# Kernel tuning notes

Hardware: AMD Instinct MI355X
Metric: run time of the kernel (lower is better)

## Reference

```python
import jax, jax.numpy as jnp
import numpy as np

B, C, H, W = 8, 128, 128, 128
C5 = 5 * C


def setup_inputs() -> dict:
    key = jax.random.key(0)
    ks = jax.random.split(key, 9)
    s_dw = 0.1   # depthwise weight scale
    s_pw = 0.02  # pointwise weight scale
    return {
        "x": jax.random.normal(ks[0], (B, C, H, W), jnp.float32),
        "w1": jax.random.normal(ks[1], (C5, 1, 1, 1), jnp.float32) * s_dw,
        "b1": jax.random.normal(ks[2], (C5,), jnp.float32) * 0.01,
        "w2": jax.random.normal(ks[3], (C5, 1, 3, 3), jnp.float32) * s_dw,
        "b2": jax.random.normal(ks[4], (C5,), jnp.float32) * 0.01,
        "w3": jax.random.normal(ks[5], (C5, 1, 3, 3), jnp.float32) * s_dw,
        "b3": jax.random.normal(ks[6], (C5,), jnp.float32) * 0.01,
        "w4": jax.random.normal(ks[7], (C, C5, 1, 1), jnp.float32) * s_pw,
        "b4": jax.random.normal(ks[8], (C,), jnp.float32) * 0.01,
    }


def nnstacking(x):
    # pad H,W by 1 then stack the 4-neighborhood + center along channels -> 5C
    p = jnp.pad(x, ((0, 0), (0, 0), (1, 1), (1, 1)))
    return jnp.concatenate(
        [p[:, :, 2:, 1:-1],   # neighbor below (i+1, j)
         p[:, :, :-2, 1:-1],  # neighbor above (i-1, j)
         p[:, :, 1:-1, 2:],   # neighbor right (i, j+1)
         p[:, :, 1:-1, :-2],  # neighbor left  (i, j-1)
         p[:, :, 1:-1, 1:-1]],  # center
        axis=1)


def _conv(x, w, b, dilation, padding, groups):
    y = jax.lax.conv_general_dilated(
        x, w, window_strides=(1, 1),
        padding=[(padding, padding), (padding, padding)],
        rhs_dilation=(dilation, dilation),
        dimension_numbers=("NCHW", "OIHW", "NCHW"),
        feature_group_count=groups)
    return y + b[None, :, None, None]


def reference(x, w1, b1, w2, b2, w3, b3, w4, b4):
    shortcut = x
    s = nnstacking(x)  # (B, 5C, H, W)
    # three depthwise branches (groups = 5C): 1x1 rate-1, 3x3 dil-8, 3x3 dil-12
    y = (_conv(s, w1, b1, 1, 0, C5)
         + _conv(s, w2, b2, 8, 8, C5)
         + _conv(s, w3, b3, 12, 12, C5))
    # pointwise 5C -> C, then residual add
    return _conv(y, w4, b4, 1, 0, 1) + shortcut
```

## Files before the change

kernel.cpp:

```cpp
#include <hip/hip_runtime.h>
#include <stdint.h>
#include <stddef.h>


static constexpr int Cc  = 128;
static constexpr int C5  = 640;
static constexpr int Hh  = 128;
static constexpr int Ww  = 128;
static constexpr int LC  = 160;
static constexpr int GR  = 48;
static constexpr int PSz = GR * LC + 8;

typedef __attribute__((ext_vector_type(8))) short short8;
typedef __attribute__((ext_vector_type(4))) float f32x4;

__device__ __forceinline__ uint16_t f2bf(float f) {
  uint32_t b = __float_as_uint(f);
  b += 0x7fffu + ((b >> 16) & 1u);
  return (uint16_t)(b >> 16);
}
__device__ __forceinline__ float bflo(uint32_t v) { return __uint_as_float(v << 16); }
__device__ __forceinline__ float bfhi(uint32_t v) { return __uint_as_float(v & 0xffff0000u); }

__device__ __forceinline__ void async16(uint16_t* lds, const uint16_t* gm) {
  __builtin_amdgcn_global_load_lds(
      (const __attribute__((address_space(1))) uint32_t*)gm,
      (__attribute__((address_space(3))) uint32_t*)lds, 16, 0, 0);
}

__global__ void prep_kernel(const float* __restrict__ w1, const float* __restrict__ b1,
                            const float* __restrict__ w2, const float* __restrict__ b2,
                            const float* __restrict__ w3, const float* __restrict__ b3,
                            const float* __restrict__ w4,
                            uint16_t* __restrict__ w4b, float* __restrict__ cw2,
                            float* __restrict__ cw3, float* __restrict__ bsum) {
  int i = blockIdx.x * 256 + threadIdx.x;
  if (i < Cc * C5) w4b[i] = f2bf(w4[i]);
  if (i < C5) {
    bsum[i] = b1[i] + b2[i] + b3[i];
#pragma unroll
    for (int t = 0; t < 9; ++t) {
      float a = w2[i * 9 + t];
      if (t == 4) a += w1[i] + w3[i * 9 + 4];
      cw2[i * 9 + t] = a;
      cw3[i * 9 + t] = w3[i * 9 + t];
    }
  }
}

__global__ __launch_bounds__(256, 2) void dw_kernel(
    const float* __restrict__ x, const float* __restrict__ cw2,
    const float* __restrict__ cw3, const float* __restrict__ bsum,
    uint16_t* __restrict__ y, int b0) {
  __shared__ uint16_t xs[4 * PSz];

  const int band = blockIdx.x;
  const int g    = blockIdx.y;
  const int bl   = blockIdx.z;
  const int bb   = b0 + bl;
  const int i0   = band * 16;
  const int tid  = threadIdx.x;

#pragma unroll
  for (int it = 0; it < 30; ++it) {
    int idx  = it * 256 + tid;
    int col4 = idx % 40;
    int rr   = (idx / 40) % 48;
    int cel  = idx / 1920;
    int gi = i0 - 16 + rr;
    int gj = col4 * 4 - 16;
    float4 v = make_float4(0.f, 0.f, 0.f, 0.f);
    if ((unsigned)gi < 128u && col4 >= 4 && col4 < 36) {
      v = *(const float4*)(x + (((size_t)(bb * Cc + g * 4 + cel) * Hh + gi) << 7) + gj);
    }
    ushort4 h;
    h.x = f2bf(v.x); h.y = f2bf(v.y); h.z = f2bf(v.z); h.w = f2bf(v.w);
    *(ushort4*)(xs + cel * PSz + rr * LC + col4 * 4) = h;
  }
  __syncthreads();

  const int ce = tid & 3;
  const int jt = (tid >> 2) & 7;
  const int ir = tid >> 5;
  const int j0 = jt * 16;
  const int c  = g * 4 + ce;

  float rb[48];
#define LOAD_RB(ROW)                                                      \
  do {                                                                    \
    const uint16_t* _p = xs + ce * PSz + (ROW) * LC + j0;                 \
    _Pragma("unroll") for (int _u = 0; _u < 6; ++_u) {                    \
      uint4 _q = *(const uint4*)(_p + _u * 8);                            \
      rb[_u * 8 + 0] = bflo(_q.x); rb[_u * 8 + 1] = bfhi(_q.x);           \
      rb[_u * 8 + 2] = bflo(_q.y); rb[_u * 8 + 3] = bfhi(_q.y);           \
      rb[_u * 8 + 4] = bflo(_q.z); rb[_u * 8 + 5] = bfhi(_q.z);           \
      rb[_u * 8 + 6] = bflo(_q.w); rb[_u * 8 + 7] = bfhi(_q.w);           \
    }                                                                     \
  } while (0)

  {
    float w2r[3][9], w3r[3][9], bs[3];
    const int msA[3] = {4, 2, 3};
#pragma unroll
    for (int mi = 0; mi < 3; ++mi) {
      int k = msA[mi] * Cc + c;
#pragma unroll
      for (int t = 0; t < 9; ++t) {
        w2r[mi][t] = cw2[k * 9 + t];
        w3r[mi][t] = cw3[k * 9 + t];
      }
      bs[mi] = bsum[k];
    }

#pragma unroll
    for (int it2 = 0; it2 < 2; ++it2) {
      const int i     = i0 + ir + 8 * it2;
      const int rbase = ir + 8 * it2 + 16;
      float acc[3][16];
#pragma unroll
      for (int mi = 0; mi < 3; ++mi)
#pragma unroll
        for (int jj = 0; jj < 16; ++jj) acc[mi][jj] = bs[mi];

#define AROW3(DLT, WARR, UB, DD)                                          \
      do {                                                                \
        LOAD_RB(rbase + (DLT));                                           \
        _Pragma("unroll") for (int mi = 0; mi < 3; ++mi) {                \
          const int aj = (mi == 0) ? 0 : ((mi == 1) ? 1 : -1);            \
          _Pragma("unroll") for (int v = 0; v < 3; ++v) {                 \
            const float w = WARR[mi][(UB) + v];                           \
            const int e = 16 + (DD) * (v - 1) + aj;                       \
            _Pragma("unroll") for (int jj = 0; jj < 16; ++jj)             \
              acc[mi][jj] += w * rb[e + jj];                              \
          }                                                               \
        }                                                                 \
      } while (0)

      AROW3(-12, w3r, 0, 12);
      if (j0 == 0)   acc[1][11] -= w3r[1][0] * rb[16];
      if (j0 == 112) acc[2][4]  -= w3r[2][2] * rb[31];

      AROW3(-8, w2r, 0, 8);
      if (j0 == 0)   acc[1][7]  -= w2r[1][0] * rb[16];
      if (j0 == 112) acc[2][8]  -= w2r[2][2] * rb[31];

      {
        LOAD_RB(rbase);
#pragma unroll
        for (int mi = 0; mi < 3; ++mi) {
          const int aj = (mi == 0) ? 0 : ((mi == 1) ? 1 : -1);
#pragma unroll
          for (int v = 0; v < 3; ++v) {
            const float w = w2r[mi][3 + v];
            const int e = 16 + 8 * (v - 1) + aj;
#pragma unroll
            for (int jj = 0; jj < 16; ++jj) acc[mi][jj] += w * rb[e + jj];
          }
          {
            const float w = w3r[mi][3]; const int e = 4 + aj;
#pragma unroll
            for (int jj = 0; jj < 16; ++jj) acc[mi][jj] += w * rb[e + jj];
          }
          {
            const float w = w3r[mi][5]; const int e = 28 + aj;
#pragma unroll
            for (int jj = 0; jj < 16; ++jj) acc[mi][jj] += w * rb[e + jj];
          }
        }
        if (j0 == 0)   { acc[1][7] -= w2r[1][3] * rb[16]; acc[1][11] -= w3r[1][3] * rb[16]; }
        if (j0 == 112) { acc[2][8] -= w2r[2][5] * rb[31]; acc[2][4]  -= w3r[2][5] * rb[31]; }
      }

      AROW3(8, w2r, 6, 8);
      if (j0 == 0)   acc[1][7]  -= w2r[1][6] * rb[16];
      if (j0 == 112) acc[2][8]  -= w2r[2][8] * rb[31];

      AROW3(12, w3r, 6, 12);
      if (j0 == 0)   acc[1][11] -= w3r[1][6] * rb[16];
      if (j0 == 112) acc[2][4]  -= w3r[2][8] * rb[31];
#undef AROW3

#pragma unroll
      for (int mi = 0; mi < 3; ++mi) {
        const int msA_[3] = {4, 2, 3};
        int k4 = msA_[mi] * 32 + g;
        size_t base = (((size_t)(bl * 160 + k4) << 14) + (size_t)i * Ww + j0) * 4 + ce;
#pragma unroll
        for (int jj = 0; jj < 16; ++jj) y[base + jj * 4] = f2bf(acc[mi][jj]);
      }
    }
  }

  {
    float w2r[2][9], w3r[2][9], bs[2];
#pragma unroll
    for (int mi = 0; mi < 2; ++mi) {
      int k = mi * Cc + c;
#pragma unroll
      for (int t = 0; t < 9; ++t) {
        w2r[mi][t] = cw2[k * 9 + t];
        w3r[mi][t] = cw3[k * 9 + t];
      }
      bs[mi] = bsum[k];
    }

#pragma unroll
    for (int it2 = 0; it2 < 2; ++it2) {
      const int i     = i0 + ir + 8 * it2;
      const int rbase = ir + 8 * it2 + 16;
      float acc[2][16];
#pragma unroll
      for (int mi = 0; mi < 2; ++mi)
#pragma unroll
        for (int jj = 0; jj < 16; ++jj) acc[mi][jj] = bs[mi];

#define BROW3(MI, DLT, WARR, UB, DD, BADROW)                              \
      do {                                                                \
        LOAD_RB(rbase + (DLT));                                           \
        const float sel = ((i + (DLT)) == (BADROW)) ? 0.f : 1.f;          \
        _Pragma("unroll") for (int v = 0; v < 3; ++v) {                   \
          const float w = WARR[MI][(UB) + v] * sel;                       \
          const int e = 16 + (DD) * (v - 1);                              \
          _Pragma("unroll") for (int jj = 0; jj < 16; ++jj)               \
            acc[MI][jj] += w * rb[e + jj];                                \
        }                                                                 \
      } while (0)

#define BROWC(MI, DLT, BADROW)                                            \
      do {                                                                \
        LOAD_RB(rbase + (DLT));                                           \
        const float sel = ((i + (DLT)) == (BADROW)) ? 0.f : 1.f;          \
        _Pragma("unroll") for (int v = 0; v < 3; ++v) {                   \
          const float w = w2r[MI][3 + v] * sel;                           \
          const int e = 16 + 8 * (v - 1);                                 \
          _Pragma("unroll") for (int jj = 0; jj < 16; ++jj)               \
            acc[MI][jj] += w * rb[e + jj];                                \
        }                                                                 \
        {                                                                 \
          const float w = w3r[MI][3] * sel;                               \
          _Pragma("unroll") for (int jj = 0; jj < 16; ++jj)               \
            acc[MI][jj] += w * rb[4 + jj];                                \
        }                                                                 \
        {                                                                 \
          const float w = w3r[MI][5] * sel;                               \
          _Pragma("unroll") for (int jj = 0; jj < 16; ++jj)               \
            acc[MI][jj] += w * rb[28 + jj];                               \
        }                                                                 \
      } while (0)

      BROW3(0, -11, w3r, 0, 12, 0);
      BROW3(0, -7,  w2r, 0, 8, 0);
      BROWC(0, 1, 0);
      BROW3(0, 9,   w2r, 6, 8, 0);
      BROW3(0, 13,  w3r, 6, 12, 0);
      BROW3(1, -13, w3r, 0, 12, 127);
      BROW3(1, -9,  w2r, 0, 8, 127);
      BROWC(1, -1, 127);
      BROW3(1, 7,   w2r, 6, 8, 127);
      BROW3(1, 11,  w3r, 6, 12, 127);
#undef BROW3
#undef BROWC

#pragma unroll
      for (int mi = 0; mi < 2; ++mi) {
        int k4 = mi * 32 + g;
        size_t base = (((size_t)(bl * 160 + k4) << 14) + (size_t)i * Ww + j0) * 4 + ce;
#pragma unroll
        for (int jj = 0; jj < 16; ++jj) y[base + jj * 4] = f2bf(acc[mi][jj]);
      }
    }
  }
#undef LOAD_RB
}

__global__ __launch_bounds__(256, 2) void gemm_kernel(
    const uint16_t* __restrict__ w4b, const uint16_t* __restrict__ y,
    const float* __restrict__ x, const float* __restrict__ b4,
    float* __restrict__ out, int b0) {
  __shared__ uint16_t As[128 * 64];
  __shared__ uint16_t Bs[16 * 128 * 4];

  const int tid  = threadIdx.x;
  const int lane = tid & 63;
  const int wave = tid >> 6;
  const int p0   = blockIdx.x * 128;
  const int bl   = blockIdx.y;
  const int bb   = b0 + bl;

  const int col = lane & 15;
  const int q   = lane >> 4;
  const int o_base = (wave >> 1) * 64;
  const int p_base = (wave & 1) * 64;

  f32x4 acc[4][4];
#pragma unroll
  for (int fm = 0; fm < 4; ++fm)
#pragma unroll
    for (int fn = 0; fn < 4; ++fn) acc[fm][fn] = (f32x4){0.f, 0.f, 0.f, 0.f};

  for (int kt = 0; kt < 10; ++kt) {
#pragma unroll
    for (int l = 0; l < 4; ++l) {
      int u  = (wave * 4 + l) * 64 + lane;
      int o  = u >> 3, ch = u & 7;
      async16(As + u * 8, w4b + (size_t)o * 640 + kt * 64 + ch * 8);
    }
#pragma unroll
    for (int l = 0; l < 4; ++l) {
      int k4t = wave * 4 + l;
      async16(Bs + (k4t * 64 + lane) * 8,
              y + (((size_t)(bl * 160 + kt * 16 + k4t) << 14) + p0) * 4 + lane * 8);
    }
    __syncthreads();

#pragma unroll
    for (int kk = 0; kk < 2; ++kk) {
      short8 af[4], bf[4];
#pragma unroll
      for (int fm = 0; fm < 4; ++fm) {
        int o = o_base + fm * 16 + col;
        af[fm] = *(const short8*)(As + o * 64 + kk * 32 + q * 8);
      }
#pragma unroll
      for (int fn = 0; fn < 4; ++fn) {
        int p = p_base + fn * 16 + col;
        union { short8 s; uint32_t u[4]; } bu;
        const uint32_t* lo = (const uint32_t*)(Bs + ((kk * 8 + 2 * q) * 128 + p) * 4);
        const uint32_t* hi = (const uint32_t*)(Bs + ((kk * 8 + 2 * q + 1) * 128 + p) * 4);
        bu.u[0] = lo[0]; bu.u[1] = lo[1]; bu.u[2] = hi[0]; bu.u[3] = hi[1];
        bf[fn] = bu.s;
      }
#pragma unroll
      for (int fm = 0; fm < 4; ++fm)
#pragma unroll
        for (int fn = 0; fn < 4; ++fn)
          acc[fm][fn] = __builtin_amdgcn_mfma_f32_16x16x32_bf16(af[fm], bf[fn], acc[fm][fn], 0, 0, 0);
    }
    __syncthreads();
  }

#pragma unroll
  for (int fm = 0; fm < 4; ++fm) {
#pragma unroll
    for (int fn = 0; fn < 4; ++fn) {
      int pg = p0 + p_base + fn * 16 + col;
#pragma unroll
      for (int r = 0; r < 4; ++r) {
        int oo = o_base + fm * 16 + q * 4 + r;
        size_t oi = ((size_t)(bb * 128 + oo) << 14) + pg;
        out[oi] = acc[fm][fn][r] + b4[oo] + x[oi];
      }
    }
  }
}

extern "C" void kernel_launch(void* const* d_in, const int* in_sizes, int n_in,
                              void* d_out, int out_size, void* d_ws, size_t ws_size,
                              hipStream_t stream) {
  const float* x  = (const float*)d_in[0];
  const float* w1 = (const float*)d_in[1];
  const float* b1 = (const float*)d_in[2];
  const float* w2 = (const float*)d_in[3];
  const float* b2 = (const float*)d_in[4];
  const float* w3 = (const float*)d_in[5];
  const float* b3 = (const float*)d_in[6];
  const float* w4 = (const float*)d_in[7];
  const float* b4 = (const float*)d_in[8];
  float* out = (float*)d_out;

  char* ws = (char*)d_ws;
  uint16_t* w4b  = (uint16_t*)ws;
  float*    cw2  = (float*)(ws + 163840);
  float*    cw3  = (float*)(ws + 186880);
  float*    bsum = (float*)(ws + 209920);
  uint16_t* y    = (uint16_t*)(ws + (1 << 20));

  const size_t per_b = (size_t)160 * 16384 * 4 * 2;
  int nbc = 4;
  while (nbc > 1 && (size_t)(1 << 20) + (size_t)nbc * per_b > ws_size) nbc >>= 1;

  hipLaunchKernelGGL(prep_kernel, dim3(320), dim3(256), 0, stream,
                     w1, b1, w2, b2, w3, b3, w4, w4b, cw2, cw3, bsum);
  for (int b0 = 0; b0 < 8; b0 += nbc) {
    int nb = (8 - b0) < nbc ? (8 - b0) : nbc;
    hipLaunchKernelGGL(dw_kernel, dim3(8, 32, nb), dim3(256), 0, stream,
                       x, cw2, cw3, bsum, y, b0);
    hipLaunchKernelGGL(gemm_kernel, dim3(128, nb), dim3(256), 0, stream,
                       w4b, y, x, b4, out, b0);
  }
}
```

Before: 339.8 us.

## Pack depthwise outputs via lane shuffles into 16-byte stores and shrink halo tile

Replaces the 16 scattered 2-byte bf16 stores per accumulator row with packed hardware bf16 conversion plus an xor-shuffle transpose across the four channel lanes, so each thread writes two 16-byte vectors. It also trims the LDS halo from 48 to 42 rows, since the needed offsets only reach -13..+13 beyond the 16-row band, which cuts LDS use and load work. Occupancy is raised to 3 blocks per CU. The shuffle transpose adds ALU and cross-lane work and may raise register pressure under the tighter launch bound.

Result: slower. 551.6 us (+62.3%).

```diff
diff --git a/kernel.cpp b/kernel.cpp
--- a/kernel.cpp
+++ b/kernel.cpp
@@ -8,7 +8,7 @@
 static constexpr int Hh  = 128;
 static constexpr int Ww  = 128;
 static constexpr int LC  = 160;
-static constexpr int GR  = 48;
+static constexpr int GR  = 42;
 static constexpr int PSz = GR * LC + 8;
 
 typedef __attribute__((ext_vector_type(8))) short short8;
@@ -22,10 +22,69 @@
 __device__ __forceinline__ float bflo(uint32_t v) { return __uint_as_float(v << 16); }
 __device__ __forceinline__ float bfhi(uint32_t v) { return __uint_as_float(v & 0xffff0000u); }
 
+__device__ __forceinline__ uint32_t cvt_pk_bf16(float a, float b) {
+  uint32_t r;
+  asm("v_cvt_pk_bf16_f32 %0, %1, %2" : "=v"(r) : "v"(a), "v"(b));
+  return r;
+}
+
 __device__ __forceinline__ void async16(uint16_t* lds, const uint16_t* gm) {
   __builtin_amdgcn_global_load_lds(
       (const __attribute__((address_space(1))) uint32_t*)gm,
       (__attribute__((address_space(3))) uint32_t*)lds, 16, 0, 0);
+}
+
+__device__ __forceinline__ void store_pack16(uint16_t* __restrict__ dst,
+                                             int ce, const float* acc) {
+  const bool odd = (ce & 1) != 0;
+  const bool hi2 = (ce & 2) != 0;
+
+  uint32_t m[8];
+#pragma unroll
+  for (int j = 0; j < 8; ++j) m[j] = cvt_pk_bf16(acc[2 * j], acc[2 * j + 1]);
+
+  uint32_t t2[8], mp[8];
+#pragma unroll
+  for (int j = 0; j < 8; ++j) t2[j] = odd ? m[(j + 2) & 7] : m[j];
+#pragma unroll
+  for (int j = 0; j < 8; ++j) mp[j] = hi2 ? t2[(j + 4) & 7] : t2[j];
+
+  uint32_t E0 = odd ? mp[6] : mp[2];
+  uint32_t E1 = odd ? mp[7] : mp[3];
+  uint32_t E2 = odd ? mp[2] : mp[6];
+  uint32_t E3 = odd ? mp[3] : mp[7];
+  uint32_t R0 = __shfl_xor((int)E0, 1);
+  uint32_t R1 = __shfl_xor((int)E1, 1);
+  uint32_t R2 = __shfl_xor((int)E2, 1);
+  uint32_t R3 = __shfl_xor((int)E3, 1);
+
+  uint32_t O[4] = {mp[0], mp[1], mp[4], mp[5]};
+  uint32_t R[4] = {R0, R1, R2, R3};
+
+  uint32_t Q[8];
+#pragma unroll
+  for (int t = 0; t < 4; ++t) {
+    uint32_t X = odd ? R[t] : O[t];
+    uint32_t Y = odd ? O[t] : R[t];
+    Q[2 * t]     = (X & 0xffffu) | (Y << 16);
+    Q[2 * t + 1] = (X >> 16) | (Y & 0xffff0000u);
+  }
+
+  uint32_t S[4];
+#pragma unroll
+  for (int t = 0; t < 4; ++t) S[t] = __shfl_xor((int)Q[4 + t], 2);
+
+  uint32_t D[8];
+#pragma unroll
+  for (int t = 0; t < 4; ++t) {
+    D[2 * t]     = hi2 ? S[t] : Q[t];
+    D[2 * t + 1] = hi2 ? Q[t] : S[t];
+  }
+
+  uint4 v0 = make_uint4(D[0], D[1], D[2], D[3]);
+  uint4 v1 = make_uint4(D[4], D[5], D[6], D[7]);
+  *(uint4*)(dst + ce * 16)     = v0;
+  *(uint4*)(dst + ce * 16 + 8) = v1;
 }
 
 __global__ void prep_kernel(const float* __restrict__ w1, const float* __restrict__ b1,
@@ -48,7 +107,7 @@
   }
 }
 
-__global__ __launch_bounds__(256, 2) void dw_kernel(
+__global__ __launch_bounds__(256, 3) void dw_kernel(
     const float* __restrict__ x, const float* __restrict__ cw2,
     const float* __restrict__ cw3, const float* __restrict__ bsum,
     uint16_t* __restrict__ y, int b0) {
@@ -62,20 +121,22 @@
   const int tid  = threadIdx.x;
 
 #pragma unroll
-  for (int it = 0; it < 30; ++it) {
-    int idx  = it * 256 + tid;
-    int col4 = idx % 40;
-    int rr   = (idx / 40) % 48;
-    int cel  = idx / 1920;
-    int gi = i0 - 16 + rr;
-    int gj = col4 * 4 - 16;
-    float4 v = make_float4(0.f, 0.f, 0.f, 0.f);
-    if ((unsigned)gi < 128u && col4 >= 4 && col4 < 36) {
-      v = *(const float4*)(x + (((size_t)(bb * Cc + g * 4 + cel) * Hh + gi) << 7) + gj);
-    }
-    ushort4 h;
-    h.x = f2bf(v.x); h.y = f2bf(v.y); h.z = f2bf(v.z); h.w = f2bf(v.w);
-    *(ushort4*)(xs + cel * PSz + rr * LC + col4 * 4) = h;
+  for (int it = 0; it < 27; ++it) {
+    int idx = it * 256 + tid;
+    if (idx < 6720) {
+      int col4 = idx % 40;
+      int rr   = (idx / 40) % 42;
+      int cel  = idx / 1680;
+      int gi = i0 - 13 + rr;
+      int gj = col4 * 4 - 16;
+      float4 v = make_float4(0.f, 0.f, 0.f, 0.f);
+      if ((unsigned)gi < 128u && col4 >= 4 && col4 < 36) {
+        v = *(const float4*)(x + (((size_t)(bb * Cc + g * 4 + cel) * Hh + gi) << 7) + gj);
+      }
+      ushort4 h;
+      h.x = f2bf(v.x); h.y = f2bf(v.y); h.z = f2bf(v.z); h.w = f2bf(v.w);
+      *(ushort4*)(xs + cel * PSz + rr * LC + col4 * 4) = h;
+    }
   }
   __syncthreads();
 
@@ -115,7 +176,7 @@
 #pragma unroll
     for (int it2 = 0; it2 < 2; ++it2) {
       const int i     = i0 + ir + 8 * it2;
-      const int rbase = ir + 8 * it2 + 16;
+      const int rbase = ir + 8 * it2 + 13;
       float acc[3][16];
 #pragma unroll
       for (int mi = 0; mi < 3; ++mi)
@@ -184,9 +245,8 @@
       for (int mi = 0; mi < 3; ++mi) {
         const int msA_[3] = {4, 2, 3};
         int k4 = msA_[mi] * 32 + g;
-        size_t base = (((size_t)(bl * 160 + k4) << 14) + (size_t)i * Ww + j0) * 4 + ce;
-#pragma unroll
-        for (int jj = 0; jj < 16; ++jj) y[base + jj * 4] = f2bf(acc[mi][jj]);
+        size_t rowb = (((size_t)(bl * 160 + k4) << 14) + (size_t)i * Ww + j0) * 4;
+        store_pack16(y + rowb, ce, acc[mi]);
       }
     }
   }
@@ -207,7 +267,7 @@
 #pragma unroll
     for (int it2 = 0; it2 < 2; ++it2) {
       const int i     = i0 + ir + 8 * it2;
-      const int rbase = ir + 8 * it2 + 16;
+      const int rbase = ir + 8 * it2 + 13;
       float acc[2][16];
 #pragma unroll
       for (int mi = 0; mi < 2; ++mi)
@@ -264,9 +324,8 @@
 #pragma unroll
       for (int mi = 0; mi < 2; ++mi) {
         int k4 = mi * 32 + g;
-        size_t base = (((size_t)(bl * 160 + k4) << 14) + (size_t)i * Ww + j0) * 4 + ce;
-#pragma unroll
-        for (int jj = 0; jj < 16; ++jj) y[base + jj * 4] = f2bf(acc[mi][jj]);
+        size_t rowb = (((size_t)(bl * 160 + k4) << 14) + (size_t)i * Ww + j0) * 4;
+        store_pack16(y + rowb, ce, acc[mi]);
       }
     }
   }
```
